# Kernel optimization log

Measured on AMD Instinct MI355X. Metric: run time of the kernel, lower is better.

## Reference

```python
import jax, jax.numpy as jnp
import numpy as np

NUM_FEATURES = 128
NUM_FILTERS = 128

def setup_inputs() -> dict:
    key = jax.random.key(0)
    k1, k2, k3, k4, k5 = jax.random.split(key, 5)
    B, N, F = 4, 2048, NUM_FEATURES
    x = jax.random.normal(k1, (B, N, F), dtype=jnp.float32)
    A = jax.random.normal(k2, (B, N, N), dtype=jnp.float32)
    # Conv1D(num_filters, kernel_size=1, use_bias=False) == per-node linear F -> filters
    W = jax.random.normal(k3, (F, NUM_FILTERS), dtype=jnp.float32) * (1.0 / np.sqrt(F))
    # self.a: Conv1D(1, kernel_size=1) with bias == linear filters -> 1 (shared for x_i and x_j)
    a_w = jax.random.normal(k4, (NUM_FILTERS, 1), dtype=jnp.float32) * (1.0 / np.sqrt(NUM_FILTERS))
    a_b = jax.random.normal(k5, (1,), dtype=jnp.float32) * 0.01
    bias = jnp.zeros((NUM_FILTERS,), dtype=jnp.float32)
    return {"x": x, "A": A, "W": W, "a_w": a_w, "a_b": a_b, "bias": bias}

def reference(x, A, W, a_w, a_b, bias):
    # project features: [B,N,F] @ [F,Ff] -> [B,N,Ff]
    h = jnp.einsum('bnf,fg->bng', x, W)
    # shared attention projection (x_i and x_j use the same layer): [B,N,1]
    s = jnp.einsum('bng,go->bno', h, a_w) + a_b
    # additive scores s_i + s_j^T -> [B,N,N]
    e = s + jnp.swapaxes(s, 1, 2)
    e = jnp.where(e >= 0, e, 0.2 * e)  # LeakyReLU(0.2)
    attn = jax.nn.softmax(e + A, axis=-1)
    out = jnp.einsum('bij,bjg->big', attn, h) + bias
    return out
```

## Files before the change

kernel.cpp:

```cpp
#include <hip/hip_runtime.h>
#include <hip/hip_bf16.h>
#include <stdint.h>

#define BB 4
#define NN 2048
#define FF 128

typedef __attribute__((ext_vector_type(8))) short bf16x8;
typedef __attribute__((ext_vector_type(4))) float f32x4;

__device__ inline unsigned pk_bf16(float a, float b) {
    union { float f; unsigned u; } x, y;
    x.f = a; y.f = b;
    unsigned xu = x.u + (0x7fffu + ((x.u >> 16) & 1u));
    unsigned yu = y.u + (0x7fffu + ((y.u >> 16) & 1u));
    return (xu >> 16) | (yu & 0xffff0000u);
}
__device__ inline uint16_t b16(float v) {
    union { float f; unsigned u; } c; c.f = v;
    return (uint16_t)((c.u + (0x7fffu + ((c.u >> 16) & 1u))) >> 16);
}
__device__ inline void glds16(const void* g, void* l) {
    __builtin_amdgcn_global_load_lds((const __attribute__((address_space(1))) void*)g,
                                     (__attribute__((address_space(3))) void*)l, 16, 0, 0);
}

#define XT_P 136
#define WT_P 136

__global__ __launch_bounds__(256) void k1_proj(
    const float* __restrict__ x, const float* __restrict__ W,
    const float* __restrict__ a_w, const float* __restrict__ a_b,
    uint16_t* __restrict__ Ht, float* __restrict__ s_out)
{
    __shared__ uint16_t xt[16 * XT_P];
    __shared__ uint16_t Wt[128 * WT_P];
    __shared__ float sredw[4 * 16];

    const int t = threadIdx.x;
    const int w = t >> 6, l = t & 63;
    const int m16 = l & 15, q = l >> 4;
    const int b = blockIdx.x >> 7;
    const int n0 = (blockIdx.x & 127) << 4;

    const int c4 = (t & 31) * 4, kh = (t >> 5) * 16;
    float4 wr0[8], wr1[8];
    #pragma unroll
    for (int kk = 0; kk < 8; ++kk) {
        const int k = kh + 2 * kk;
        wr0[kk] = *(const float4*)(W + (size_t)k * 128 + c4);
        wr1[kk] = *(const float4*)(W + (size_t)(k + 1) * 128 + c4);
    }
    {
        const int row = t >> 4, c0 = (t & 15) * 8;
        const float* xr = x + ((size_t)(b * NN + n0 + row)) * FF + c0;
        const float4 v0 = *(const float4*)xr;
        const float4 v1 = *(const float4*)(xr + 4);
        unsigned* dst = (unsigned*)(xt + row * XT_P + c0);
        dst[0] = pk_bf16(v0.x, v0.y); dst[1] = pk_bf16(v0.z, v0.w);
        dst[2] = pk_bf16(v1.x, v1.y); dst[3] = pk_bf16(v1.z, v1.w);
    }
    #pragma unroll
    for (int kk = 0; kk < 8; ++kk) {
        const int k = kh + 2 * kk;
        *(unsigned*)(Wt + (c4 + 0) * WT_P + k) = pk_bf16(wr0[kk].x, wr1[kk].x);
        *(unsigned*)(Wt + (c4 + 1) * WT_P + k) = pk_bf16(wr0[kk].y, wr1[kk].y);
        *(unsigned*)(Wt + (c4 + 2) * WT_P + k) = pk_bf16(wr0[kk].z, wr1[kk].z);
        *(unsigned*)(Wt + (c4 + 3) * WT_P + k) = pk_bf16(wr0[kk].w, wr1[kk].w);
    }
    const int g0 = (2 * w) * 16 + m16, g1 = (2 * w + 1) * 16 + m16;
    const float aw0 = a_w[g0], aw1 = a_w[g1];
    __syncthreads();

    f32x4 acc0 = {}, acc1 = {};
    bf16x8 af[4];
    #pragma unroll
    for (int dk = 0; dk < 4; ++dk)
        af[dk] = *(const bf16x8*)(xt + m16 * XT_P + dk * 32 + q * 8);
    #pragma unroll
    for (int dk = 0; dk < 4; ++dk) {
        bf16x8 b0 = *(const bf16x8*)(Wt + g0 * WT_P + dk * 32 + q * 8);
        bf16x8 b1 = *(const bf16x8*)(Wt + g1 * WT_P + dk * 32 + q * 8);
        acc0 = __builtin_amdgcn_mfma_f32_16x16x32_bf16(af[dk], b0, acc0, 0, 0, 0);
        acc1 = __builtin_amdgcn_mfma_f32_16x16x32_bf16(af[dk], b1, acc1, 0, 0, 0);
    }

    float sp[4];
    #pragma unroll
    for (int r = 0; r < 4; ++r) sp[r] = acc0[r] * aw0 + acc1[r] * aw1;
    #pragma unroll
    for (int off = 1; off < 16; off <<= 1)
        #pragma unroll
        for (int r = 0; r < 4; ++r) sp[r] += __shfl_xor(sp[r], off, 64);
    if (m16 == 0) {
        #pragma unroll
        for (int r = 0; r < 4; ++r) sredw[w * 16 + q * 4 + r] = sp[r];
    }
    {
        uint2 o0 = { pk_bf16(acc0[0], acc0[1]), pk_bf16(acc0[2], acc0[3]) };
        uint2 o1 = { pk_bf16(acc1[0], acc1[1]), pk_bf16(acc1[2], acc1[3]) };
        *(uint2*)(Ht + ((size_t)(b * 128 + g0)) * NN + n0 + q * 4) = o0;
        *(uint2*)(Ht + ((size_t)(b * 128 + g1)) * NN + n0 + q * 4) = o1;
    }
    __syncthreads();
    if (t < 16)
        s_out[b * NN + n0 + t] = sredw[t] + sredw[16 + t] + sredw[32 + t] + sredw[48 + t] + a_b[0];
}

#define JS 8
#define JRR 256
#define NRND 16

__global__ __launch_bounds__(256) void k2_attn(
    const float* __restrict__ A, const uint16_t* __restrict__ Ht,
    const float* __restrict__ s, uint16_t* __restrict__ po,
    float* __restrict__ prs)
{
    __shared__ uint16_t hts[128 * 256];
    __shared__ float abuf[2][16 * 256];
    __shared__ uint16_t pbuf[16 * 256];
    __shared__ float rsLds[256];
    __shared__ float sLds[256];

    const int t = threadIdx.x;
    const int w = t >> 6, l = t & 63;
    const int m16 = l & 15, q = l >> 4;
    const int x7 = m16 & 7;

    const int bx = blockIdx.x;
    const int is = bx & 7;
    const int js = (bx >> 3) & 7;
    const int b  = bx >> 6;
    const int j0 = js * JRR;
    const int i0 = is * 256;

    const float* sb = s + b * NN;
    const float* Ab = A + (size_t)b * NN * NN;
    const uint16_t* Hb = Ht + (size_t)b * FF * NN;

    const int jA = 2 * w * 32 + q * 8;
    float4 sj0 = *(const float4*)(sb + j0 + jA);
    float4 sj1 = *(const float4*)(sb + j0 + jA + 4);
    float4 sj2 = *(const float4*)(sb + j0 + jA + 32);
    float4 sj3 = *(const float4*)(sb + j0 + jA + 36);

    #pragma unroll
    for (int u = 0; u < 16; ++u) {
        const int row = 32 * w + 2 * u + (l >> 5);
        const int c = l & 31;
        glds16(Hb + (size_t)row * NN + j0 + 8 * (c ^ (row & 7)),
               hts + (32 * w + 2 * u) * 256);
    }
    #pragma unroll
    for (int u = 0; u < 4; ++u) {
        const int row = 4 * w + u;
        glds16(Ab + (size_t)(i0 + row) * NN + j0 + 4 * (l ^ (row & 7)),
               &abuf[0][row * 256]);
    }
    if (w == 0) glds16(sb + i0 + l * 4, sLds);
    __syncthreads();

    for (int r = 0; r < NRND; ++r) {
        const int cur = r & 1, nxt = cur ^ 1;
        const int rn = (r + 1) & (NRND - 1);

        #pragma unroll
        for (int u = 0; u < 4; ++u) {
            const int row = 4 * w + u;
            glds16(Ab + (size_t)(i0 + rn * 16 + row) * NN + j0 + 4 * (l ^ (row & 7)),
                   &abuf[nxt][row * 256]);
        }
        asm volatile("s_waitcnt vmcnt(13)\n\ts_barrier" ::: "memory");

        const float si = sLds[r * 16 + m16];

        const int ga0 = (2 * w) * 8 + 2 * q;
        const int ga1 = (2 * w + 1) * 8 + 2 * q;
        const float* ac = &abuf[cur][m16 * 256];
        float4 a0 = *(const float4*)(ac + 4 * (ga0 ^ x7));
        float4 a1 = *(const float4*)(ac + 4 * ((ga0 + 1) ^ x7));
        float4 a2 = *(const float4*)(ac + 4 * (ga1 ^ x7));
        float4 a3 = *(const float4*)(ac + 4 * ((ga1 + 1) ^ x7));

        const float sv[16] = {sj0.x,sj0.y,sj0.z,sj0.w, sj1.x,sj1.y,sj1.z,sj1.w,
                              sj2.x,sj2.y,sj2.z,sj2.w, sj3.x,sj3.y,sj3.z,sj3.w};
        const float av[16] = {a0.x,a0.y,a0.z,a0.w, a1.x,a1.y,a1.z,a1.w,
                              a2.x,a2.y,a2.z,a2.w, a3.x,a3.y,a3.z,a3.w};
        float pv[16]; float rs = 0.f;
        #pragma unroll
        for (int j = 0; j < 16; ++j) {
            float e = si + sv[j];
            e = fmaxf(e, 0.2f * e);
            pv[j] = __expf(e + av[j]);
            rs += pv[j];
        }
        union { unsigned u[4]; bf16x8 v; } pk0, pk1;
        #pragma unroll
        for (int j = 0; j < 4; ++j) {
            pk0.u[j] = pk_bf16(pv[2 * j], pv[2 * j + 1]);
            pk1.u[j] = pk_bf16(pv[8 + 2 * j], pv[9 + 2 * j]);
        }
        *(bf16x8*)(pbuf + m16 * 256 + 8 * ((8 * w + q) ^ x7)) = pk0.v;
        *(bf16x8*)(pbuf + m16 * 256 + 8 * ((8 * w + 4 + q) ^ x7)) = pk1.v;
        rsLds[t] = rs;
        asm volatile("s_waitcnt lgkmcnt(0)\n\ts_barrier" ::: "memory");

        f32x4 acc0 = {}, acc1 = {};
        const int gA = w * 32 + m16, gB = w * 32 + 16 + m16;
        #pragma unroll
        for (int kk = 0; kk < 8; ++kk) {
            const int jc = kk * 4 + q;
            bf16x8 af = *(const bf16x8*)(pbuf + m16 * 256 + 8 * (jc ^ x7));
            bf16x8 h0 = *(const bf16x8*)(hts + gA * 256 + 8 * (jc ^ x7));
            bf16x8 h1 = *(const bf16x8*)(hts + gB * 256 + 8 * (jc ^ x7));
            acc0 = __builtin_amdgcn_mfma_f32_16x16x32_bf16(af, h0, acc0, 0, 0, 0);
            acc1 = __builtin_amdgcn_mfma_f32_16x16x32_bf16(af, h1, acc1, 0, 0, 0);
        }

        if (l < 16) {
            float sum = 0.f;
            #pragma unroll
            for (int w2 = 0; w2 < 4; ++w2)
                #pragma unroll
                for (int q2 = 0; q2 < 4; ++q2)
                    sum += rsLds[w2 * 64 + q2 * 16 + l];
            prs[(size_t)(js * BB + b) * NN + i0 + r * 16 + l] = sum;
        }

        const size_t pob = ((size_t)(js * BB + b) * NN + i0 + r * 16) * FF;
        #pragma unroll
        for (int rr = 0; rr < 4; ++rr) {
            const int irow = q * 4 + rr;
            po[pob + (size_t)irow * FF + w * 32 + m16]      = b16(acc0[rr]);
            po[pob + (size_t)irow * FF + w * 32 + 16 + m16] = b16(acc1[rr]);
        }
        asm volatile("s_waitcnt lgkmcnt(0)\n\ts_barrier" ::: "memory");
    }
}

__global__ __launch_bounds__(256) void k3_red(
    const uint16_t* __restrict__ po, const float* __restrict__ prs,
    const float* __restrict__ bias, float* __restrict__ out)
{
    const int idx = blockIdx.x * 256 + threadIdx.x;
    const int g = idx & 127;
    const int i = (idx >> 7) & (NN - 1);
    const int b = idx >> 18;
    float sum = 0.f, rsum = 0.f;
    #pragma unroll
    for (int js = 0; js < JS; ++js) {
        const size_t base = (size_t)(js * BB + b) * NN + i;
        union { unsigned u; float f; } cv;
        cv.u = ((unsigned)po[base * FF + g]) << 16;
        sum += cv.f;
        rsum += prs[base];
    }
    out[idx] = sum / rsum + bias[g];
}

extern "C" void kernel_launch(void* const* d_in, const int* in_sizes, int n_in,
                              void* d_out, int out_size, void* d_ws, size_t ws_size,
                              hipStream_t stream) {
    const float* x    = (const float*)d_in[0];
    const float* A    = (const float*)d_in[1];
    const float* W    = (const float*)d_in[2];
    const float* a_w  = (const float*)d_in[3];
    const float* a_b  = (const float*)d_in[4];
    const float* bias = (const float*)d_in[5];
    float* out = (float*)d_out;

    char* ws = (char*)d_ws;
    uint16_t* Ht = (uint16_t*)ws;
    float* s = (float*)(ws + 2 * 1024 * 1024);
    uint16_t* po = (uint16_t*)(ws + 2 * 1024 * 1024 + 65536);
    float* prs = (float*)(ws + 2 * 1024 * 1024 + 65536 + (size_t)JS * BB * NN * FF * 2);

    k1_proj<<<BB * (NN / 16), 256, 0, stream>>>(x, W, a_w, a_b, Ht, s);
    k2_attn<<<BB * 8 * 8, 256, 0, stream>>>(A, Ht, s, po, prs);
    k3_red<<<(BB * NN * FF) / 256, 256, 0, stream>>>(po, prs, bias, out);
}
```

Before: 135.0 us.

## Keep H fragments in registers and split j across waves in attention kernel

```diff
diff --git a/kernel.cpp b/kernel.cpp
--- a/kernel.cpp
+++ b/kernel.cpp
@@ -15,14 +15,6 @@
     unsigned xu = x.u + (0x7fffu + ((x.u >> 16) & 1u));
     unsigned yu = y.u + (0x7fffu + ((y.u >> 16) & 1u));
     return (xu >> 16) | (yu & 0xffff0000u);
-}
-__device__ inline uint16_t b16(float v) {
-    union { float f; unsigned u; } c; c.f = v;
-    return (uint16_t)((c.u + (0x7fffu + ((c.u >> 16) & 1u))) >> 16);
-}
-__device__ inline void glds16(const void* g, void* l) {
-    __builtin_amdgcn_global_load_lds((const __attribute__((address_space(1))) void*)g,
-                                     (__attribute__((address_space(3))) void*)l, 16, 0, 0);
 }
 
 #define XT_P 136
@@ -108,133 +100,124 @@
 }
 
 #define JS 8
-#define JRR 256
-#define NRND 16
-
-__global__ __launch_bounds__(256) void k2_attn(
+#define IRND 8
+
+__global__ __launch_bounds__(256, 2) void k2_attn(
     const float* __restrict__ A, const uint16_t* __restrict__ Ht,
     const float* __restrict__ s, uint16_t* __restrict__ po,
     float* __restrict__ prs)
 {
-    __shared__ uint16_t hts[128 * 256];
-    __shared__ float abuf[2][16 * 256];
-    __shared__ uint16_t pbuf[16 * 256];
-    __shared__ float rsLds[256];
-    __shared__ float sLds[256];
+    __shared__ float Opw[4][16 * 132];
+    __shared__ float rsw[4][16];
 
     const int t = threadIdx.x;
     const int w = t >> 6, l = t & 63;
     const int m16 = l & 15, q = l >> 4;
-    const int x7 = m16 & 7;
 
     const int bx = blockIdx.x;
-    const int is = bx & 7;
-    const int js = (bx >> 3) & 7;
-    const int b  = bx >> 6;
-    const int j0 = js * JRR;
-    const int i0 = is * 256;
+    const int js = bx & 7;
+    const int is = (bx >> 3) & 15;
+    const int b  = bx >> 7;
+    const int j0 = js * 256;
+    const int ibase = is * 128;
 
     const float* sb = s + b * NN;
     const float* Ab = A + (size_t)b * NN * NN;
     const uint16_t* Hb = Ht + (size_t)b * FF * NN;
 
-    const int jA = 2 * w * 32 + q * 8;
-    float4 sj0 = *(const float4*)(sb + j0 + jA);
-    float4 sj1 = *(const float4*)(sb + j0 + jA + 4);
-    float4 sj2 = *(const float4*)(sb + j0 + jA + 32);
-    float4 sj3 = *(const float4*)(sb + j0 + jA + 36);
-
-    #pragma unroll
-    for (int u = 0; u < 16; ++u) {
-        const int row = 32 * w + 2 * u + (l >> 5);
-        const int c = l & 31;
-        glds16(Hb + (size_t)row * NN + j0 + 8 * (c ^ (row & 7)),
-               hts + (32 * w + 2 * u) * 256);
-    }
-    #pragma unroll
-    for (int u = 0; u < 4; ++u) {
-        const int row = 4 * w + u;
-        glds16(Ab + (size_t)(i0 + row) * NN + j0 + 4 * (l ^ (row & 7)),
-               &abuf[0][row * 256]);
-    }
-    if (w == 0) glds16(sb + i0 + l * 4, sLds);
-    __syncthreads();
-
-    for (int r = 0; r < NRND; ++r) {
-        const int cur = r & 1, nxt = cur ^ 1;
-        const int rn = (r + 1) & (NRND - 1);
-
-        #pragma unroll
-        for (int u = 0; u < 4; ++u) {
-            const int row = 4 * w + u;
-            glds16(Ab + (size_t)(i0 + rn * 16 + row) * NN + j0 + 4 * (l ^ (row & 7)),
-                   &abuf[nxt][row * 256]);
-        }
-        asm volatile("s_waitcnt vmcnt(13)\n\ts_barrier" ::: "memory");
-
-        const float si = sLds[r * 16 + m16];
-
-        const int ga0 = (2 * w) * 8 + 2 * q;
-        const int ga1 = (2 * w + 1) * 8 + 2 * q;
-        const float* ac = &abuf[cur][m16 * 256];
-        float4 a0 = *(const float4*)(ac + 4 * (ga0 ^ x7));
-        float4 a1 = *(const float4*)(ac + 4 * ((ga0 + 1) ^ x7));
-        float4 a2 = *(const float4*)(ac + 4 * (ga1 ^ x7));
-        float4 a3 = *(const float4*)(ac + 4 * ((ga1 + 1) ^ x7));
-
-        const float sv[16] = {sj0.x,sj0.y,sj0.z,sj0.w, sj1.x,sj1.y,sj1.z,sj1.w,
-                              sj2.x,sj2.y,sj2.z,sj2.w, sj3.x,sj3.y,sj3.z,sj3.w};
-        const float av[16] = {a0.x,a0.y,a0.z,a0.w, a1.x,a1.y,a1.z,a1.w,
-                              a2.x,a2.y,a2.z,a2.w, a3.x,a3.y,a3.z,a3.w};
+    const int jc0 = j0 + w * 32 + q * 8;
+    const int jc1 = j0 + (w + 4) * 32 + q * 8;
+
+    float4 sj00 = *(const float4*)(sb + jc0);
+    float4 sj01 = *(const float4*)(sb + jc0 + 4);
+    float4 sj10 = *(const float4*)(sb + jc1);
+    float4 sj11 = *(const float4*)(sb + jc1 + 4);
+
+    bf16x8 hf0[8], hf1[8];
+    #pragma unroll
+    for (int gt = 0; gt < 8; ++gt) {
+        const uint16_t* hp = Hb + (size_t)(gt * 16 + m16) * NN;
+        hf0[gt] = *(const bf16x8*)(hp + jc0);
+        hf1[gt] = *(const bf16x8*)(hp + jc1);
+    }
+
+    const float* Ar = Ab + (size_t)(ibase + m16) * NN;
+    float4 a00 = *(const float4*)(Ar + jc0);
+    float4 a01 = *(const float4*)(Ar + jc0 + 4);
+    float4 a10 = *(const float4*)(Ar + jc1);
+    float4 a11 = *(const float4*)(Ar + jc1 + 4);
+    float si = sb[ibase + m16];
+
+    const size_t slice = (size_t)(js * BB + b);
+
+    for (int r = 0; r < IRND; ++r) {
+        const int i0r = ibase + r * 16;
+        const int i0n = ibase + ((r + 1) & (IRND - 1)) * 16;
+
+        const float* An = Ab + (size_t)(i0n + m16) * NN;
+        float4 n00 = *(const float4*)(An + jc0);
+        float4 n01 = *(const float4*)(An + jc0 + 4);
+        float4 n10 = *(const float4*)(An + jc1);
+        float4 n11 = *(const float4*)(An + jc1 + 4);
+        const float sin_ = sb[i0n + m16];
+
+        const float svv[16] = {sj00.x,sj00.y,sj00.z,sj00.w, sj01.x,sj01.y,sj01.z,sj01.w,
+                               sj10.x,sj10.y,sj10.z,sj10.w, sj11.x,sj11.y,sj11.z,sj11.w};
+        const float avv[16] = {a00.x,a00.y,a00.z,a00.w, a01.x,a01.y,a01.z,a01.w,
+                               a10.x,a10.y,a10.z,a10.w, a11.x,a11.y,a11.z,a11.w};
         float pv[16]; float rs = 0.f;
         #pragma unroll
         for (int j = 0; j < 16; ++j) {
-            float e = si + sv[j];
+            float e = si + svv[j];
             e = fmaxf(e, 0.2f * e);
-            pv[j] = __expf(e + av[j]);
+            pv[j] = __expf(e + avv[j]);
             rs += pv[j];
         }
-        union { unsigned u[4]; bf16x8 v; } pk0, pk1;
+        union { unsigned u[4]; bf16x8 v; } fa0, fa1;
         #pragma unroll
         for (int j = 0; j < 4; ++j) {
-            pk0.u[j] = pk_bf16(pv[2 * j], pv[2 * j + 1]);
-            pk1.u[j] = pk_bf16(pv[8 + 2 * j], pv[9 + 2 * j]);
-        }
-        *(bf16x8*)(pbuf + m16 * 256 + 8 * ((8 * w + q) ^ x7)) = pk0.v;
-        *(bf16x8*)(pbuf + m16 * 256 + 8 * ((8 * w + 4 + q) ^ x7)) = pk1.v;
-        rsLds[t] = rs;
+            fa0.u[j] = pk_bf16(pv[2 * j], pv[2 * j + 1]);
+            fa1.u[j] = pk_bf16(pv[8 + 2 * j], pv[9 + 2 * j]);
+        }
+
+        f32x4 acc[8];
+        #pragma unroll
+        for (int gt = 0; gt < 8; ++gt) {
+            f32x4 z = {0.f, 0.f, 0.f, 0.f};
+            z = __builtin_amdgcn_mfma_f32_16x16x32_bf16(fa0.v, hf0[gt], z, 0, 0, 0);
+            acc[gt] = __builtin_amdgcn_mfma_f32_16x16x32_bf16(fa1.v, hf1[gt], z, 0, 0, 0);
+        }
+
+        rs += __shfl_xor(rs, 16, 64);
+        rs += __shfl_xor(rs, 32, 64);
+        if (q == 0) rsw[w][m16] = rs;
+
+        #pragma unroll
+        for (int gt = 0; gt < 8; ++gt)
+            #pragma unroll
+            for (int rr = 0; rr < 4; ++rr)
+                Opw[w][(q * 4 + rr) * 132 + gt * 16 + m16] = acc[gt][rr];
         asm volatile("s_waitcnt lgkmcnt(0)\n\ts_barrier" ::: "memory");
 
-        f32x4 acc0 = {}, acc1 = {};
-        const int gA = w * 32 + m16, gB = w * 32 + 16 + m16;
-        #pragma unroll
-        for (int kk = 0; kk < 8; ++kk) {
-            const int jc = kk * 4 + q;
-            bf16x8 af = *(const bf16x8*)(pbuf + m16 * 256 + 8 * (jc ^ x7));
-            bf16x8 h0 = *(const bf16x8*)(hts + gA * 256 + 8 * (jc ^ x7));
-            bf16x8 h1 = *(const bf16x8*)(hts + gB * 256 + 8 * (jc ^ x7));
-            acc0 = __builtin_amdgcn_mfma_f32_16x16x32_bf16(af, h0, acc0, 0, 0, 0);
-            acc1 = __builtin_amdgcn_mfma_f32_16x16x32_bf16(af, h1, acc1, 0, 0, 0);
-        }
-
-        if (l < 16) {
-            float sum = 0.f;
+        {
+            const int row = t >> 4, k8 = (t & 15) * 8;
+            float v[8] = {0.f,0.f,0.f,0.f,0.f,0.f,0.f,0.f};
             #pragma unroll
-            for (int w2 = 0; w2 < 4; ++w2)
-                #pragma unroll
-                for (int q2 = 0; q2 < 4; ++q2)
-                    sum += rsLds[w2 * 64 + q2 * 16 + l];
-            prs[(size_t)(js * BB + b) * NN + i0 + r * 16 + l] = sum;
-        }
-
-        const size_t pob = ((size_t)(js * BB + b) * NN + i0 + r * 16) * FF;
-        #pragma unroll
-        for (int rr = 0; rr < 4; ++rr) {
-            const int irow = q * 4 + rr;
-            po[pob + (size_t)irow * FF + w * 32 + m16]      = b16(acc0[rr]);
-            po[pob + (size_t)irow * FF + w * 32 + 16 + m16] = b16(acc1[rr]);
+            for (int sl = 0; sl < 4; ++sl) {
+                float4 u0 = *(const float4*)&Opw[sl][row * 132 + k8];
+                float4 u1 = *(const float4*)&Opw[sl][row * 132 + k8 + 4];
+                v[0] += u0.x; v[1] += u0.y; v[2] += u0.z; v[3] += u0.w;
+                v[4] += u1.x; v[5] += u1.y; v[6] += u1.z; v[7] += u1.w;
+            }
+            unsigned* op = (unsigned*)(po + ((slice * NN + i0r + row) * FF + k8));
+            op[0] = pk_bf16(v[0], v[1]); op[1] = pk_bf16(v[2], v[3]);
+            op[2] = pk_bf16(v[4], v[5]); op[3] = pk_bf16(v[6], v[7]);
+            if (t < 16)
+                prs[slice * NN + i0r + t] = rsw[0][t] + rsw[1][t] + rsw[2][t] + rsw[3][t];
         }
         asm volatile("s_waitcnt lgkmcnt(0)\n\ts_barrier" ::: "memory");
+
+        a00 = n00; a01 = n01; a10 = n10; a11 = n11; si = sin_;
     }
 }
 
@@ -276,6 +259,6 @@
     float* prs = (float*)(ws + 2 * 1024 * 1024 + 65536 + (size_t)JS * BB * NN * FF * 2);
 
     k1_proj<<<BB * (NN / 16), 256, 0, stream>>>(x, W, a_w, a_b, Ht, s);
-    k2_attn<<<BB * 8 * 8, 256, 0, stream>>>(A, Ht, s, po, prs);
+    k2_attn<<<JS * 16 * BB, 256, 0, stream>>>(A, Ht, s, po, prs);
     k3_red<<<(BB * NN * FF) / 256, 256, 0, stream>>>(po, prs, bias, out);
 }
```

Measured after the change: 124.9 us. 7.4% less time.
